# Optimization experiments

Measured on AMD Instinct MI355X. Metric: run time of the kernel, lower is better.

Reference implementation:

```python
import jax, jax.numpy as jnp
from jax import lax
import numpy as np

# static config matching init_kwargs
PROPOSAL_COUNT = 1000
NMS_THRESH = 0.7
MIN_SIZE = 16.0
IMG_H, IMG_W = 512, 512
NUM_ANCHORS = 262144
BATCH = 16
PRE_NMS = min(6000, NUM_ANCHORS)


def setup_inputs() -> dict:
    key = jax.random.key(0)
    k1, k2, k3, k4, k5 = jax.random.split(key, 5)
    # realistic anchors: centers uniform in image, sizes in [16, 160]
    cx = jax.random.uniform(k1, (NUM_ANCHORS,), minval=0.0, maxval=float(IMG_W))
    cy = jax.random.uniform(k2, (NUM_ANCHORS,), minval=0.0, maxval=float(IMG_H))
    w = jax.random.uniform(k3, (NUM_ANCHORS,), minval=16.0, maxval=160.0)
    h = jax.random.uniform(k4, (NUM_ANCHORS,), minval=16.0, maxval=160.0)
    anchors = jnp.stack([cx - 0.5 * w, cy - 0.5 * h, cx + 0.5 * w, cy + 0.5 * h], axis=1)
    ka, kb = jax.random.split(k5)
    rpn_class_probs = jax.random.uniform(ka, (BATCH, NUM_ANCHORS, 2), dtype=jnp.float32)
    rpn_bbox_deltas = jax.random.normal(kb, (BATCH, NUM_ANCHORS, 4), dtype=jnp.float32) * 0.2
    return {"anchors": anchors, "rpn_class_probs": rpn_class_probs, "rpn_bbox_deltas": rpn_bbox_deltas}


def apply_box_deltas(anchors, deltas):
    # standard (dx, dy, dw, dh) decode in center form
    w = anchors[:, 2] - anchors[:, 0]
    h = anchors[:, 3] - anchors[:, 1]
    cx = anchors[:, 0] + 0.5 * w
    cy = anchors[:, 1] + 0.5 * h
    cx = cx + deltas[:, 0] * w
    cy = cy + deltas[:, 1] * h
    w = w * jnp.exp(deltas[:, 2])
    h = h * jnp.exp(deltas[:, 3])
    return jnp.stack([cx - 0.5 * w, cy - 0.5 * h, cx + 0.5 * w, cy + 0.5 * h], axis=1)


def nms_keep(boxes, valid):
    # greedy NMS over score-sorted boxes [n,4]; invalid boxes start suppressed
    x1, y1, x2, y2 = boxes[:, 0], boxes[:, 1], boxes[:, 2], boxes[:, 3]
    areas = (x2 - x1) * (y2 - y1)
    n = boxes.shape[0]

    def body(i, state):
        suppressed, keep = state
        is_valid = jnp.logical_not(suppressed[i])
        keep = keep.at[i].set(is_valid)
        xx1 = jnp.maximum(x1[i], x1)
        yy1 = jnp.maximum(y1[i], y1)
        xx2 = jnp.minimum(x2[i], x2)
        yy2 = jnp.minimum(y2[i], y2)
        inter = jnp.maximum(xx2 - xx1, 0.0) * jnp.maximum(yy2 - yy1, 0.0)
        iou = inter / (areas[i] + areas - inter + 1e-9)
        iou = iou.at[i].set(0.0)  # never self-suppress
        suppressed = suppressed | (is_valid & (iou > NMS_THRESH))
        return suppressed, keep

    suppressed0 = jnp.logical_not(valid)
    keep0 = jnp.zeros((n,), dtype=bool)
    _, keep = lax.fori_loop(0, n, body, (suppressed0, keep0))
    return keep


def _per_image(scores, deltas, anchors):
    boxes = apply_box_deltas(anchors, deltas)
    boxes = jnp.stack([
        jnp.clip(boxes[:, 0], 0.0, IMG_W - 1.0),
        jnp.clip(boxes[:, 1], 0.0, IMG_H - 1.0),
        jnp.clip(boxes[:, 2], 0.0, IMG_W - 1.0),
        jnp.clip(boxes[:, 3], 0.0, IMG_H - 1.0),
    ], axis=1)
    ws = boxes[:, 2] - boxes[:, 0]
    hs = boxes[:, 3] - boxes[:, 1]
    valid = (ws >= MIN_SIZE) & (hs >= MIN_SIZE)
    # emulate boolean filter + descending sort with fixed shapes:
    # invalid boxes get -inf score so they sort to the back and start suppressed.
    masked = jnp.where(valid, scores, -jnp.inf)
    order = jnp.argsort(-masked)[:PRE_NMS]
    boxes_s = boxes[order]
    valid_s = valid[order]
    keep = nms_keep(lax.stop_gradient(boxes_s), valid_s)
    idx = jnp.flatnonzero(keep, size=PROPOSAL_COUNT, fill_value=PRE_NMS)
    boxes_pad = jnp.concatenate([boxes_s, jnp.zeros((1, 4), boxes_s.dtype)], axis=0)
    return boxes_pad[idx]  # [proposal_count, 4], zero-padded like torch


def reference(anchors, rpn_class_probs, rpn_bbox_deltas):
    fg_scores = rpn_class_probs[:, :, 1]
    return jax.vmap(_per_image, in_axes=(0, 0, None))(fg_scores, rpn_bbox_deltas, anchors)
```

## Files before the change

### kernel.cpp

```cpp
#include <hip/hip_runtime.h>
#include <cstdint>

#define B 16
#define N 262144
#define PRE 6000
#define KOUT 1000
#define MW 94
#define CW 24
#define NOFF 276
#define NJOB 576
#define ECAP 4096
#define RMAX 64
#define NBIN 2049
#define PREFILT 1967
#define PGATE 0.9599609375f
#define IMGMAX 511.0f
#define NMS_TH 0.7f

typedef unsigned int u32;
typedef unsigned long long u64;

#define OFF_MASK  0ull
#define OFF_SEL   72192000ull
#define OFF_BOX   74289152ull
#define OFF_VAL   75829248ull
#define OFF_HIST  75841536ull
#define OFF_CAB   75972864ull
#define OFF_BCNT  76104192ull
#define OFF_T     76235520ull
#define OFF_M     76235584ull
#define OFF_FLAG  76235648ull
#define OFF_ECNT  76235712ull
#define OFF_EDG   76235776ull
#define OFF_DW    76497920ull
#define OFF_PL    76825600ull
#define OFF_PCNT  78922752ull
#define WS_NEED   78922816ull

__device__ __forceinline__ void box_from(const float4 a, const float4 d,
    float& x1, float& y1, float& x2, float& y2, bool& valid) {
#pragma clang fp contract(off)
  float w  = a.z - a.x;
  float h  = a.w - a.y;
  float cx = a.x + 0.5f * w;
  float cy = a.y + 0.5f * h;
  cx = cx + d.x * w;
  cy = cy + d.y * h;
  w = w * expf(d.z);
  h = h * expf(d.w);
  x1 = cx - 0.5f * w;
  y1 = cy - 0.5f * h;
  x2 = cx + 0.5f * w;
  y2 = cy + 0.5f * h;
  x1 = fminf(fmaxf(x1, 0.0f), IMGMAX);
  y1 = fminf(fmaxf(y1, 0.0f), IMGMAX);
  x2 = fminf(fmaxf(x2, 0.0f), IMGMAX);
  y2 = fminf(fmaxf(y2, 0.0f), IMGMAX);
  valid = ((x2 - x1) >= 16.0f) && ((y2 - y1) >= 16.0f);
}

__device__ __forceinline__ bool iou_gt(float inter, float denom) {
  float d = inter - NMS_TH * denom;
  if (__builtin_expect(fabsf(d) <= 1e-4f * denom, 0))
    return (inter / denom) > NMS_TH;
  return d > 0.0f;
}

__device__ __forceinline__ int bin_of(u32 u) {
  if (u == 0u) return 0;
  float s = __uint_as_float(u & 0x7FFFFFFFu);
  return 1 + min(2047, (int)(s * 2048.0f));
}

__global__ void k_hist(const float4* __restrict__ anch, const float2* __restrict__ probs,
                       const float4* __restrict__ delt, u32* __restrict__ hist,
                       float4* __restrict__ boxes, u64* __restrict__ plist,
                       u32* __restrict__ pcnt) {
  __shared__ u32 sh[128];
  __shared__ u64 qbuf[192];
  __shared__ u64 pbuf[256];
  __shared__ u32 qcl, pcl, pbase;
  int t = threadIdx.x;
  int img = blockIdx.y;
  if (t == 0) { qcl = 0; pcl = 0; }
  if (blockIdx.x == 0 && t < 16)
    boxes[(size_t)img * 6016 + 6000 + t] = make_float4(0.f, 0.f, 0.f, 0.f);
  if (t < 128) sh[t] = 0;
  __syncthreads();
  const float4* pr4 = (const float4*)(probs + (size_t)img * N);
  int b4 = blockIdx.x * 1024 + t;
  float4 p0 = pr4[b4];
  float4 p1 = pr4[b4 + 256];
  float4 p2 = pr4[b4 + 512];
  float4 p3 = pr4[b4 + 768];
  auto check = [&](float s, int i) {
    if (s >= PGATE) {
      u32 q = atomicAdd(&qcl, 1u);
      if (q < 192u)
        qbuf[q] = ((u64)__float_as_uint(s) << 32) | (u64)(u32)i;
    }
  };
  check(p0.y, 2 * b4);            check(p0.w, 2 * b4 + 1);
  check(p1.y, 2 * (b4 + 256));    check(p1.w, 2 * (b4 + 256) + 1);
  check(p2.y, 2 * (b4 + 512));    check(p2.w, 2 * (b4 + 512) + 1);
  check(p3.y, 2 * (b4 + 768));    check(p3.w, 2 * (b4 + 768) + 1);
  __syncthreads();
  u32 qn = min(qcl, 192u);
  for (u32 q = t; q < qn; q += 256) {
    u64 qv = qbuf[q];
    float s = __uint_as_float((u32)(qv >> 32));
    int i = (int)(u32)qv;
    float4 a = anch[i];
    float4 d = delt[(size_t)img * N + i];
    float x1, y1, x2, y2; bool valid;
    box_from(a, d, x1, y1, x2, y2, valid);
    if (valid) {
      int bin = 1 + min(2047, (int)(s * 2048.0f));
      atomicAdd(&sh[bin - 1921], 1u);
      u64 key = ((u64)(__float_as_uint(s) | 0x80000000u) << 32)
              | (u64)(0xFFFFFFFFu - (u32)i);
      u32 p = atomicAdd(&pcl, 1u);
      if (p < 256u) pbuf[p] = key;
    }
  }
  __syncthreads();
  if (t < 128 && sh[t]) atomicAdd(&hist[img * 2052 + 1921 + t], sh[t]);
  u32 n = min(pcl, 256u);
  if (t == 0) {
    if (qcl > 192u || pcl > 256u)
      atomicAdd(&pcnt[img], 1000000u);
    pbase = n ? atomicAdd(&pcnt[img], n) : 0u;
  }
  __syncthreads();
  for (u32 p = t; p < n; p += 256) {
    u32 dp = pbase + p;
    if (dp < 16384u) plist[(size_t)img * 16384 + dp] = pbuf[p];
  }
}

__global__ void k_thresh(const u32* __restrict__ hist, int* __restrict__ Tarr,
                         u32* __restrict__ cab, u32* __restrict__ Marr) {
  int img = blockIdx.x;
  int l = threadIdx.x;
  const u32* hb = hist + img * 2052;
  u32 v0 = hb[1921 + 2 * l];
  u32 v1 = hb[1922 + 2 * l];
  u32 csum = v0 + v1;
  u32 sfx = csum;
  for (int off = 1; off < 64; off <<= 1) {
    u32 tv = __shfl_down(sfx, off);
    if (l + off < 64) sfx += tv;
  }
  u32 excl = sfx - csum;
  u32* cb = cab + img * 2052;
  cb[1921 + 2 * l] = excl + v1;
  cb[1922 + 2 * l] = excl;
  u32 sfxP = __shfl(excl, 22);
  bool ok = (sfxP >= (u32)PRE);
  if (l == 0 && !ok) { Tarr[img] = -1; Marr[img] = 0; }
  if (ok && excl < (u32)PRE && sfx >= (u32)PRE) {
    int T; u32 M;
    if (excl + v1 >= (u32)PRE) { T = 1922 + 2 * l; M = excl + v1; }
    else                       { T = 1921 + 2 * l; M = sfx; }
    Tarr[img] = T; Marr[img] = M;
  }
}

__global__ void k_hist_fb(const float4* __restrict__ anch, const float2* __restrict__ probs,
                          const float4* __restrict__ delt, const int* __restrict__ Tarr,
                          u32* __restrict__ hist) {
  int img = blockIdx.y;
  if (Tarr[img] >= 0) return;
  __shared__ u32 sh[NBIN];
  int t = threadIdx.x;
  for (int p = t; p < NBIN; p += 256) sh[p] = 0;
  __syncthreads();
  int base = blockIdx.x * 1024;
  for (int r = 0; r < 4; r++) {
    int i = base + r * 256 + t;
    float4 a = anch[i];
    float4 d = delt[(size_t)img * N + i];
    float s = probs[(size_t)img * N + i].y;
    float x1, y1, x2, y2; bool valid;
    box_from(a, d, x1, y1, x2, y2, valid);
    int bin = valid ? (1 + min(2047, (int)(s * 2048.0f))) : 0;
    if (bin < PREFILT) atomicAdd(&sh[bin], 1u);
  }
  __syncthreads();
  for (int p = t; p < NBIN; p += 256)
    if (sh[p]) atomicAdd(&hist[img * 2052 + p], sh[p]);
}

__global__ void k_thresh_fb(const u32* __restrict__ hist, int* __restrict__ Tarr,
                            u32* __restrict__ cab, u32* __restrict__ Marr) {
  int img = blockIdx.x;
  if (Tarr[img] >= 0) return;
  int l = threadIdx.x;
  const u32* hb = hist + img * 2052;
  u32 v[32];
  u32 csum = 0;
#pragma unroll
  for (int k = 0; k < 32; k++) { v[k] = hb[l * 32 + 1 + k]; csum += v[k]; }
  u32 sfx = csum;
  for (int off = 1; off < 64; off <<= 1) {
    u32 tv = __shfl_down(sfx, off);
    if (l + off < 64) sfx += tv;
  }
  u32 excl = sfx - csum;
  u32 ss = 0;
  u32 outv[32];
#pragma unroll
  for (int k = 31; k >= 0; k--) { outv[k] = ss + excl; ss += v[k]; }
  u32* cb = cab + img * 2052;
#pragma unroll
  for (int k = 0; k < 32; k++) cb[l * 32 + 1 + k] = outv[k];
  u32 total = __shfl(sfx, 0);
  if (l == 0) cb[0] = total;
  if (l == 0 && total < PRE) { Tarr[img] = 0; Marr[img] = 16384u; }
  if (excl < PRE && sfx >= PRE) {
    u32 acc = excl; int T = 0; u32 Mv = 0;
#pragma unroll
    for (int k = 31; k >= 0; k--) {
      acc += v[k];
      if (acc >= PRE) { T = l * 32 + 1 + k; Mv = acc; break; }
    }
    Tarr[img] = T; Marr[img] = Mv;
  }
}

__global__ void k_compact_fast(const u64* __restrict__ plist, const u32* __restrict__ pcnt,
                               const int* __restrict__ Tarr, const u32* __restrict__ cab,
                               u32* __restrict__ bincnt, u64* __restrict__ sel) {
  int t = threadIdx.x, img = blockIdx.y;
  int T = Tarr[img];
  u32 P = pcnt[img];
  if (T < PREFILT || P > 16384u) return;
  const u32* cb = cab + img * 2052;
  for (u32 i = blockIdx.x * 256u + (u32)t; i < P; i += 8u * 256u) {
    u64 key = plist[(size_t)img * 16384 + i];
    int bin = bin_of((u32)(key >> 32));
    if (bin >= T) {
      u32 p = atomicAdd(&bincnt[img * 2052 + bin], 1u);
      u32 dst = cb[bin] + p;
      if (dst < 16384u) sel[(size_t)img * 16384 + dst] = key;
    }
  }
}

__global__ void k_compact_fb(const float4* __restrict__ anch, const float2* __restrict__ probs,
                             const float4* __restrict__ delt, const u32* __restrict__ pcnt,
                             const int* __restrict__ Tarr, const u32* __restrict__ cab,
                             u32* __restrict__ bincnt, u64* __restrict__ sel) {
  int t = threadIdx.x, img = blockIdx.y;
  int T = Tarr[img];
  u32 P = pcnt[img];
  if (T >= PREFILT && P <= 16384u) return;
  const u32* cb = cab + img * 2052;
  for (int chunk = 0; chunk < 32; chunk++) {
    int i = (blockIdx.x * 32 + chunk) * 256 + t;
    float4 a = anch[i];
    float4 d = delt[(size_t)img * N + i];
    float s = probs[(size_t)img * N + i].y;
    float x1, y1, x2, y2; bool valid;
    box_from(a, d, x1, y1, x2, y2, valid);
    int bin = valid ? (1 + min(2047, (int)(s * 2048.0f))) : 0;
    if (bin >= T) {
      u64 key = ((u64)(valid ? (__float_as_uint(s) | 0x80000000u) : 0u) << 32)
              | (u64)(0xFFFFFFFFu - (u32)i);
      u32 p = atomicAdd(&bincnt[img * 2052 + bin], 1u);
      u32 dst = cb[bin] + p;
      if (dst < 16384u) sel[(size_t)img * 16384 + dst] = key;
    }
  }
}

__global__ void k_rank(const u64* __restrict__ sel, const u32* __restrict__ cab,
                       const u32* __restrict__ hist, const u32* __restrict__ Marr,
                       const float4* __restrict__ anch, const float4* __restrict__ delt,
                       float4* __restrict__ boxes, u64* __restrict__ validw) {
  int t = threadIdx.x, img = blockIdx.y;
  u32 M = min(Marr[img], 16384u);
  u32 ci = blockIdx.x * 256u + (u32)t;
  if (ci >= M) return;
  const u64* sb = sel + (size_t)img * 16384;
  u64 key = sb[ci];
  u32 u = (u32)(key >> 32);
  int bin = bin_of(u);
  const u32* cb = cab + img * 2052;
  u32 segs = cb[bin];
  u32 sege;
  if (bin > 0) sege = cb[bin - 1];
  else         sege = min(16384u, segs + hist[img * 2052 + 0]);
  if (sege > 16384u) sege = 16384u;
  u32 within = 0;
  u32 j = segs;
  for (; j + 4 <= sege; j += 4) {
    within += (sb[j]     > key);
    within += (sb[j + 1] > key);
    within += (sb[j + 2] > key);
    within += (sb[j + 3] > key);
  }
  for (; j < sege; j++) within += (sb[j] > key);
  u32 rank = segs + within;
  if (rank < PRE) {
    u32 gi = 0xFFFFFFFFu - (u32)(key & 0xFFFFFFFFull);
    float4 a = anch[gi];
    float4 d = delt[(size_t)img * N + gi];
    float x1, y1, x2, y2; bool valid;
    box_from(a, d, x1, y1, x2, y2, valid);
    boxes[(size_t)img * 6016 + rank] = make_float4(x1, y1, x2, y2);
    if (u != 0u)
      atomicOr(&validw[img * 96 + (rank >> 6)], 1ull << (rank & 63));
  }
}

__global__ void __launch_bounds__(256) k_mask(
    const float4* __restrict__ boxes, u64* __restrict__ dwbuf,
    u32* __restrict__ ecnt, u32* __restrict__ edges) {
  __shared__ float4 cbox[4][64];
  __shared__ float  carea[4][64];
  __shared__ u32 ebuf[4][128];
  __shared__ u32 ecl[4], ebase[4];
  int t = threadIdx.x;
  int l = t & 63, w = t >> 6;
  int img = blockIdx.y;
  int jid = blockIdx.x * 4 + w;
  bool diag = (jid < CW);
  int rb, cb, half = 0, nc;
  if (diag) { rb = cb = jid; nc = 64; }
  else {
    int k = jid - CW;
    int oid = k >> 1;
    half = k & 1;
    int r0 = (int)((47.0f - sqrtf((float)(47 * 47 - 8 * oid))) * 0.5f);
    if (r0 < 0) r0 = 0;
    if (r0 > CW - 2) r0 = CW - 2;
    while (r0 > 0 && ((r0 * (47 - r0)) >> 1) > oid) r0--;
    while ((((r0 + 1) * (46 - r0)) >> 1) <= oid) r0++;
    rb = r0;
    cb = rb + 1 + (oid - ((rb * (47 - rb)) >> 1));
    nc = 32;
  }
  if (l == 0) ecl[w] = 0;
  const float4* bb = boxes + (size_t)img * 6016;
  int r = rb * 64 + l;
  float4 rx = bb[r];
  float ra = (rx.z - rx.x) * (rx.w - rx.y);
  int colbase = cb * 64 + half * 32;
  if (l < nc) {
    float4 c = bb[colbase + l];
    cbox[w][l] = c;
    carea[w][l] = (c.z - c.x) * (c.w - c.y);
  }
  __syncthreads();
  if (diag) {
    u64 bits = 0ull;
    {
#pragma clang fp contract(off)
#pragma unroll 8
      for (int m = 0; m < 64; m++) {
        float4 cx = cbox[w][m];
        float xx1 = fmaxf(rx.x, cx.x);
        float yy1 = fmaxf(rx.y, cx.y);
        float xx2 = fminf(rx.z, cx.z);
        float yy2 = fminf(rx.w, cx.w);
        float inter = fmaxf(xx2 - xx1, 0.0f) * fmaxf(yy2 - yy1, 0.0f);
        float denom = ra + carea[w][m] - inter + 1e-9f;
        if (iou_gt(inter, denom) && m != l) bits |= (1ull << m);
      }
    }
    dwbuf[((size_t)img * CW + cb) * 64 + l] = bits;
  } else {
    {
#pragma clang fp contract(off)
#pragma unroll 8
      for (int m = 0; m < 32; m++) {
        float4 cx = cbox[w][m];
        float xx1 = fmaxf(rx.x, cx.x);
        float yy1 = fmaxf(rx.y, cx.y);
        float xx2 = fminf(rx.z, cx.z);
        float yy2 = fminf(rx.w, cx.w);
        float inter = fmaxf(xx2 - xx1, 0.0f) * fmaxf(yy2 - yy1, 0.0f);
        float denom = ra + carea[w][m] - inter + 1e-9f;
        if (__builtin_expect(iou_gt(inter, denom), 0)) {
          u32 p = atomicAdd(&ecl[w], 1u);
          if (p < 128u) ebuf[w][p] = (((u32)(colbase + m)) << 16) | (u32)r;
        }
      }
    }
    asm volatile("" ::: "memory");
    u32 n = ecl[w];
    if (n == 0u) return;
    if (n > 128u) n = 128u;
    if (l == 0) {
      if (ecl[w] > 128u) atomicAdd(&ecnt[img], 1000000u);
      ebase[w] = atomicAdd(&ecnt[img], n);
    }
    asm volatile("" ::: "memory");
    u32 eb0 = ebase[w];
    for (u32 p = l; p < n; p += 64) {
      u32 dp = eb0 + p;
      if (dp < ECAP) edges[(size_t)img * ECAP + dp] = ebuf[w][p];
    }
  }
}

__global__ void k_mask_rest(const float4* __restrict__ boxes, u64* __restrict__ mask,
                            const u32* __restrict__ okf) {
  int rb = blockIdx.x, img = blockIdx.y;
  if (okf[img]) return;
  __shared__ float4 cbox[4][64];
  __shared__ float  carea[4][64];
  int t = threadIdx.x;
  int rl = t & 63, g = t >> 6;
  const float4* bb = boxes + (size_t)img * 6016;
  int r = rb * 64 + rl;
  float4 rx = bb[r];
  float ra = (rx.z - rx.x) * (rx.w - rx.y);
  u64* mimg = mask + (size_t)img * 94 * 6000;
  int cb0 = rb;
  int jmax = (94 - cb0 + 3) >> 2;
  for (int j = 0; j < jmax; j++) {
    int cb = cb0 + g + 4 * j;
    bool act = cb < 94;
    __syncthreads();
    if (act) {
      float4 c = bb[cb * 64 + rl];
      cbox[g][rl] = c;
      carea[g][rl] = (c.z - c.x) * (c.w - c.y);
    }
    __syncthreads();
    if (act) {
#pragma clang fp contract(off)
      u64 bits = 0ull;
      for (int m = 0; m < 64; m++) {
        float4 cx = cbox[g][m];
        float xx1 = fmaxf(rx.x, cx.x);
        float yy1 = fmaxf(rx.y, cx.y);
        float xx2 = fminf(rx.z, cx.z);
        float yy2 = fminf(rx.w, cx.w);
        float inter = fmaxf(xx2 - xx1, 0.0f) * fmaxf(yy2 - yy1, 0.0f);
        float denom = ra + carea[g][m] - inter + 1e-9f;
        int c_j = cb * 64 + m;
        if (iou_gt(inter, denom) && c_j != r) bits |= (1ull << m);
      }
      if (r < PRE) mimg[(size_t)cb * 6000 + r] = bits;
    }
  }
}

__global__ void __launch_bounds__(64, 1) k_scan_fast(
    const u64* __restrict__ dwbuf, const u64* __restrict__ validw,
    const float4* __restrict__ boxes, float4* __restrict__ out,
    u32* __restrict__ okf, const u32* __restrict__ ecnt,
    const u32* __restrict__ edges) {
  __shared__ u64 dw[CW * 64];
  __shared__ u64 al[CW], fw[CW], kp[CW], blkX[CW], supX[CW];
  __shared__ u32 eb[ECAP];
  __shared__ unsigned short list[KOUT];
  int l = threadIdx.x;
  int img = blockIdx.x;
  for (int c = 0; c < CW; c++)
    dw[c * 64 + l] = dwbuf[((size_t)img * CW + c) * 64 + l];
  u32 E = ecnt[img];
  if (E > (u32)ECAP) { if (l == 0) okf[img] = 0u; return; }
  for (u32 p = l; p < E; p += 64) eb[p] = edges[(size_t)img * ECAP + p];
  if (l < CW) {
    al[l] = validw[img * 96 + l];
    kp[l] = 0ull; blkX[l] = 0ull; supX[l] = 0ull;
  }
  __syncthreads();
  u64 lmask = (1ull << l) - 1ull;
  bool fail = false;
  for (int round = 0; ; round++) {
    u64 anyv = (l < CW) ? al[l] : 0ull;
#pragma unroll
    for (int off = 32; off >= 1; off >>= 1) anyv |= __shfl_xor(anyv, off);
    if (anyv == 0ull) break;
    if (round >= RMAX) { fail = true; break; }
    for (u32 p = l; p < E; p += 64) {
      u32 e = eb[p];
      u32 tgt = e >> 16, src = e & 0xFFFFu;
      if ((al[src >> 6] >> (src & 63u)) & 1ull)
        atomicOr(&blkX[tgt >> 6], 1ull << (tgt & 63u));
    }
    for (int c = 0; c < CW; c++) {
      u64 a_c = al[c];
      u64 dj = dw[c * 64 + l];
      u64 blkin = __ballot((dj & a_c & lmask) != 0ull);
      if (l == 0) fw[c] = a_c & ~blkin & ~blkX[c];
    }
    for (u32 p = l; p < E; p += 64) {
      u32 e = eb[p];
      u32 tgt = e >> 16, src = e & 0xFFFFu;
      if ((fw[src >> 6] >> (src & 63u)) & 1ull)
        atomicOr(&supX[tgt >> 6], 1ull << (tgt & 63u));
    }
    for (int c = 0; c < CW; c++) {
      u64 f_c = fw[c];
      u64 dj = dw[c * 64 + l];
      u64 supin = __ballot((dj & f_c & lmask) != 0ull);
      if (l == 0) {
        kp[c] |= f_c;
        al[c] = al[c] & ~f_c & ~supin & ~supX[c];
      }
    }
    if (l < CW) { blkX[l] = 0ull; supX[l] = 0ull; }
  }
  u64 kw_l = (!fail && l < CW) ? kp[l] : 0ull;
  u32 pc = (u32)__popcll(kw_l);
  u32 pre = pc;
  for (int off = 1; off < 64; off <<= 1) {
    u32 v2 = __shfl_up(pre, off);
    if (l >= off) pre += v2;
  }
  u32 tot = __shfl(pre, 63);
  bool ok = !fail && (tot >= (u32)KOUT);
  if (l == 0) okf[img] = ok ? 1u : 0u;
  if (!ok) return;
  if (l < CW) {
    u32 b = pre - pc;
    u64 word = kw_l;
    while (word && b < (u32)KOUT) {
      int j = (int)__ffsll(word) - 1;
      word &= word - 1;
      list[b++] = (unsigned short)(l * 64 + j);
    }
  }
  __syncthreads();
  for (int p = l; p < KOUT; p += 64)
    out[(size_t)img * KOUT + p] = boxes[(size_t)img * 6016 + list[p]];
}

__global__ void k_scan_full(const u64* __restrict__ mask, const u64* __restrict__ validw,
                            const float4* __restrict__ boxes, float4* __restrict__ out,
                            const u32* __restrict__ okf) {
  int img = blockIdx.x;
  if (okf[img]) return;
  __shared__ unsigned short kept[KOUT];
  int l = threadIdx.x;
  const u64* vw = validw + img * 96;
  u64 r0 = ~vw[l];
  u64 r1 = (l < MW - 64) ? ~vw[64 + l] : ~0ull;
  const u64* c0p = mask + ((size_t)img * 94 + l) * 6000;
  const u64* c1p = mask + ((size_t)img * 94 + (l < MW - 64 ? 64 + l : 0)) * 6000;

  u64 ca[16], cb[16], na[16], nb2[16];
#pragma unroll
  for (int k = 0; k < 16; k++) {
    ca[k] = c0p[k];
    cb[k] = (l < MW - 64) ? c1p[k] : 0ull;
  }
  int cnt = 0; bool done = false;
  for (int base = 0; base < PRE; base += 16) {
#pragma unroll
    for (int k = 0; k < 16; k++) {
      int rr = base + 16 + k;
      if (rr < PRE) {
        na[k]  = c0p[rr];
        nb2[k] = (l < MW - 64) ? c1p[rr] : 0ull;
      } else { na[k] = 0ull; nb2[k] = 0ull; }
    }
#pragma unroll
    for (int k = 0; k < 16; k++) {
      if (!done) {
        int i = base + k;
        int w = i >> 6;
        u64 wv = (w < 64) ? __shfl(r0, w) : __shfl(r1, w - 64);
        if (!((wv >> (i & 63)) & 1ull)) {
          if (l == 0 && cnt < KOUT) kept[cnt] = (unsigned short)i;
          cnt++;
          r0 |= (l >= w)        ? ca[k] : 0ull;
          r1 |= ((64 + l) >= w) ? cb[k] : 0ull;
          if (cnt >= KOUT) done = true;
        }
      }
    }
    if (done) break;
#pragma unroll
    for (int k = 0; k < 16; k++) { ca[k] = na[k]; cb[k] = nb2[k]; }
  }
  __syncthreads();
  for (int p = l; p < KOUT; p += 64) {
    float4 v = make_float4(0.f, 0.f, 0.f, 0.f);
    if (p < cnt) v = boxes[(size_t)img * 6016 + kept[p]];
    out[(size_t)img * KOUT + p] = v;
  }
}

extern "C" void kernel_launch(void* const* d_in, const int* in_sizes, int n_in,
                              void* d_out, int out_size, void* d_ws, size_t ws_size,
                              hipStream_t stream) {
  const float4* anch  = (const float4*)d_in[0];
  const float2* probs = (const float2*)d_in[1];
  const float4* delt  = (const float4*)d_in[2];
  float4* out = (float4*)d_out;
  char* ws = (char*)d_ws;
  (void)in_sizes; (void)n_in;

  if (ws_size < WS_NEED) {
    (void)hipMemsetAsync(d_out, 0, (size_t)out_size * sizeof(float), stream);
    return;
  }

  u64* mask    = (u64*)(ws + OFF_MASK);
  u64* sel     = (u64*)(ws + OFF_SEL);
  float4* bxs  = (float4*)(ws + OFF_BOX);
  u64* validw  = (u64*)(ws + OFF_VAL);
  u32* hist    = (u32*)(ws + OFF_HIST);
  u32* cab     = (u32*)(ws + OFF_CAB);
  u32* bincnt  = (u32*)(ws + OFF_BCNT);
  int* Tarr    = (int*)(ws + OFF_T);
  u32* Marr    = (u32*)(ws + OFF_M);
  u32* okf     = (u32*)(ws + OFF_FLAG);
  u32* ecnt    = (u32*)(ws + OFF_ECNT);
  u32* edges   = (u32*)(ws + OFF_EDG);
  u64* dwbuf   = (u64*)(ws + OFF_DW);
  u64* plist   = (u64*)(ws + OFF_PL);
  u32* pcnt    = (u32*)(ws + OFF_PCNT);

  (void)hipMemsetAsync(ws + OFF_VAL, 0, 406528, stream);
  (void)hipMemsetAsync(ws + OFF_PCNT, 0, 64, stream);

  dim3 g1h(128, B);
  k_hist<<<g1h, 256, 0, stream>>>(anch, probs, delt, hist, bxs, plist, pcnt);
  k_thresh<<<B, 64, 0, stream>>>(hist, Tarr, cab, Marr);
  dim3 g1(256, B);
  k_hist_fb<<<g1, 256, 0, stream>>>(anch, probs, delt, Tarr, hist);
  k_thresh_fb<<<B, 64, 0, stream>>>(hist, Tarr, cab, Marr);
  dim3 g3(8, B);
  k_compact_fast<<<g3, 256, 0, stream>>>(plist, pcnt, Tarr, cab, bincnt, sel);
  dim3 g3b(32, B);
  k_compact_fb<<<g3b, 256, 0, stream>>>(anch, probs, delt, pcnt, Tarr, cab, bincnt, sel);
  dim3 g4(64, B);
  k_rank<<<g4, 256, 0, stream>>>(sel, cab, hist, Marr, anch, delt, bxs, validw);
  dim3 g5(NJOB / 4, B);
  k_mask<<<g5, 256, 0, stream>>>(bxs, dwbuf, ecnt, edges);
  k_scan_fast<<<B, 64, 0, stream>>>(dwbuf, validw, bxs, out, okf, ecnt, edges);
  dim3 g5b(94, B);
  k_mask_rest<<<g5b, 256, 0, stream>>>(bxs, mask, okf);
  k_scan_full<<<B, 64, 0, stream>>>(mask, validw, bxs, out, okf);
}
```

Measured before the change: 167.8 us.

## Assign one 64x64 IoU tile per block, splitting columns across four waves

The first-pass mask kernel now gives each block one upper-triangular 64x64 tile (300 tiles), with the four waves each handling 16 columns, where before each wave handled its own diagonal tile or half off-diagonal tile. Diagonal tiles combine the per-wave bit masks through shared memory, and off-diagonal tiles collect edges in one shared buffer per block with a single global atomic. This shortens each thread's serial loop and spreads work more evenly, at the cost of extra block syncs and more blocks to launch.

```diff
diff --git a/kernel.cpp b/kernel.cpp
--- a/kernel.cpp
+++ b/kernel.cpp
@@ -7,8 +7,7 @@
 #define KOUT 1000
 #define MW 94
 #define CW 24
-#define NOFF 276
-#define NJOB 576
+#define NTILE 300
 #define ECAP 4096
 #define RMAX 64
 #define NBIN 2049
@@ -317,90 +316,88 @@
 __global__ void __launch_bounds__(256) k_mask(
     const float4* __restrict__ boxes, u64* __restrict__ dwbuf,
     u32* __restrict__ ecnt, u32* __restrict__ edges) {
-  __shared__ float4 cbox[4][64];
-  __shared__ float  carea[4][64];
-  __shared__ u32 ebuf[4][128];
-  __shared__ u32 ecl[4], ebase[4];
+  __shared__ float4 cbox[64];
+  __shared__ float  carea[64];
+  __shared__ u64 pb[4][64];
+  __shared__ u32 ebuf[256];
+  __shared__ u32 ecl, ebase;
   int t = threadIdx.x;
   int l = t & 63, w = t >> 6;
   int img = blockIdx.y;
-  int jid = blockIdx.x * 4 + w;
-  bool diag = (jid < CW);
-  int rb, cb, half = 0, nc;
-  if (diag) { rb = cb = jid; nc = 64; }
-  else {
-    int k = jid - CW;
-    int oid = k >> 1;
-    half = k & 1;
-    int r0 = (int)((47.0f - sqrtf((float)(47 * 47 - 8 * oid))) * 0.5f);
-    if (r0 < 0) r0 = 0;
-    if (r0 > CW - 2) r0 = CW - 2;
-    while (r0 > 0 && ((r0 * (47 - r0)) >> 1) > oid) r0--;
-    while ((((r0 + 1) * (46 - r0)) >> 1) <= oid) r0++;
-    rb = r0;
-    cb = rb + 1 + (oid - ((rb * (47 - rb)) >> 1));
-    nc = 32;
-  }
-  if (l == 0) ecl[w] = 0;
+  int tid = blockIdx.x;
+  float disc = (float)((2 * CW + 1) * (2 * CW + 1) - 8 * tid);
+  int rb = (int)(((float)(2 * CW + 1) - sqrtf(disc)) * 0.5f);
+  if (rb < 0) rb = 0;
+  if (rb > CW - 1) rb = CW - 1;
+  while (rb > 0 && (rb * CW - (rb * (rb - 1)) / 2) > tid) rb--;
+  while (((rb + 1) * CW - ((rb + 1) * rb) / 2) <= tid) rb++;
+  int cb = rb + (tid - (rb * CW - (rb * (rb - 1)) / 2));
+  if (t == 0) ecl = 0;
   const float4* bb = boxes + (size_t)img * 6016;
+  if (t < 64) {
+    float4 c = bb[cb * 64 + t];
+    cbox[t] = c;
+    carea[t] = (c.z - c.x) * (c.w - c.y);
+  }
+  __syncthreads();
   int r = rb * 64 + l;
   float4 rx = bb[r];
   float ra = (rx.z - rx.x) * (rx.w - rx.y);
-  int colbase = cb * 64 + half * 32;
-  if (l < nc) {
-    float4 c = bb[colbase + l];
-    cbox[w][l] = c;
-    carea[w][l] = (c.z - c.x) * (c.w - c.y);
-  }
-  __syncthreads();
+  bool diag = (cb == rb);
+  int c0 = w * 16;
   if (diag) {
     u64 bits = 0ull;
     {
 #pragma clang fp contract(off)
-#pragma unroll 8
-      for (int m = 0; m < 64; m++) {
-        float4 cx = cbox[w][m];
+#pragma unroll
+      for (int mm = 0; mm < 16; mm++) {
+        int m = c0 + mm;
+        float4 cx = cbox[m];
         float xx1 = fmaxf(rx.x, cx.x);
         float yy1 = fmaxf(rx.y, cx.y);
         float xx2 = fminf(rx.z, cx.z);
         float yy2 = fminf(rx.w, cx.w);
         float inter = fmaxf(xx2 - xx1, 0.0f) * fmaxf(yy2 - yy1, 0.0f);
-        float denom = ra + carea[w][m] - inter + 1e-9f;
+        float denom = ra + carea[m] - inter + 1e-9f;
         if (iou_gt(inter, denom) && m != l) bits |= (1ull << m);
       }
     }
-    dwbuf[((size_t)img * CW + cb) * 64 + l] = bits;
+    pb[w][l] = bits;
+    __syncthreads();
+    if (t < 64)
+      dwbuf[((size_t)img * CW + cb) * 64 + t] =
+          pb[0][t] | pb[1][t] | pb[2][t] | pb[3][t];
   } else {
     {
 #pragma clang fp contract(off)
-#pragma unroll 8
-      for (int m = 0; m < 32; m++) {
-        float4 cx = cbox[w][m];
+#pragma unroll
+      for (int mm = 0; mm < 16; mm++) {
+        int m = c0 + mm;
+        float4 cx = cbox[m];
         float xx1 = fmaxf(rx.x, cx.x);
         float yy1 = fmaxf(rx.y, cx.y);
         float xx2 = fminf(rx.z, cx.z);
         float yy2 = fminf(rx.w, cx.w);
         float inter = fmaxf(xx2 - xx1, 0.0f) * fmaxf(yy2 - yy1, 0.0f);
-        float denom = ra + carea[w][m] - inter + 1e-9f;
+        float denom = ra + carea[m] - inter + 1e-9f;
         if (__builtin_expect(iou_gt(inter, denom), 0)) {
-          u32 p = atomicAdd(&ecl[w], 1u);
-          if (p < 128u) ebuf[w][p] = (((u32)(colbase + m)) << 16) | (u32)r;
+          u32 p = atomicAdd(&ecl, 1u);
+          if (p < 256u) ebuf[p] = (((u32)(cb * 64 + m)) << 16) | (u32)r;
         }
       }
     }
-    asm volatile("" ::: "memory");
-    u32 n = ecl[w];
-    if (n == 0u) return;
-    if (n > 128u) n = 128u;
-    if (l == 0) {
-      if (ecl[w] > 128u) atomicAdd(&ecnt[img], 1000000u);
-      ebase[w] = atomicAdd(&ecnt[img], n);
-    }
-    asm volatile("" ::: "memory");
-    u32 eb0 = ebase[w];
-    for (u32 p = l; p < n; p += 64) {
-      u32 dp = eb0 + p;
-      if (dp < ECAP) edges[(size_t)img * ECAP + dp] = ebuf[w][p];
+    __syncthreads();
+    u32 n = min(ecl, 256u);
+    if (n != 0u) {
+      if (t == 0) {
+        if (ecl > 256u) atomicAdd(&ecnt[img], 1000000u);
+        ebase = atomicAdd(&ecnt[img], n);
+      }
+      __syncthreads();
+      for (u32 p = t; p < n; p += 256) {
+        u32 dp = ebase + p;
+        if (dp < ECAP) edges[(size_t)img * ECAP + dp] = ebuf[p];
+      }
     }
   }
 }
@@ -634,7 +631,7 @@
   k_compact_fb<<<g3b, 256, 0, stream>>>(anch, probs, delt, pcnt, Tarr, cab, bincnt, sel);
   dim3 g4(64, B);
   k_rank<<<g4, 256, 0, stream>>>(sel, cab, hist, Marr, anch, delt, bxs, validw);
-  dim3 g5(NJOB / 4, B);
+  dim3 g5(NTILE, B);
   k_mask<<<g5, 256, 0, stream>>>(bxs, dwbuf, ecnt, edges);
   k_scan_fast<<<B, 64, 0, stream>>>(dwbuf, validw, bxs, out, okf, ecnt, edges);
   dim3 g5b(94, B);
```

Result: faster. 158.4 us (-5.6%).
